# Optimization experiments

Measured on AMD Instinct MI355X. Metric: run time of the kernel, lower is better.

Reference implementation:

```python
import jax, jax.numpy as jnp
import numpy as np

N_LAYERS = 2  # config['layer']
U_, L_, T_, A_ = 200000, 20000, 48, 2000
D_, D3_ = 96, 32
NNZ_ = 2_000_000


def _spmm(rows, cols, vals, x, n_rows):
    # y = A @ x for COO sparse A of shape [n_rows, n_cols]; x: [n_cols, d]
    return jax.ops.segment_sum(vals[:, None] * x[cols], rows, num_segments=n_rows)


def _attn_fuse(z, W1, b1, w2):
    # Attention module: project = Linear(d3,d3)+Tanh+Linear(d3,1, no bias)
    # z: [N, C, d3]; softmax over the C fused channels (dim=1)
    w = jnp.tanh(z @ W1 + b1) @ w2            # [N, C, 1]
    beta = jax.nn.softmax(w, axis=1)
    return jnp.sum(beta * z, axis=1)          # [N, d3]


def setup_inputs() -> dict:
    key = jax.random.key(0)
    ks = iter(jax.random.split(key, 64))
    inp = {}
    inp['user_emb'] = jax.random.normal(next(ks), (U_, D_), jnp.float32) * 0.1
    inp['loc_emb'] = jax.random.normal(next(ks), (L_, D3_), jnp.float32) * 0.1
    inp['time_emb'] = jax.random.normal(next(ks), (T_, D3_), jnp.float32) * 0.1
    inp['act_emb'] = jax.random.normal(next(ks), (A_, D3_), jnp.float32) * 0.1
    for f in ('l', 't', 'a'):
        s = 1.0 / np.sqrt(D3_)
        inp[f'W1_{f}'] = jax.random.normal(next(ks), (D3_, D3_), jnp.float32) * s
        inp[f'b1_{f}'] = jnp.zeros((D3_,), jnp.float32)
        inp[f'w2_{f}'] = jax.random.normal(next(ks), (D3_, 1), jnp.float32) * s

    def add_sparse(prefix, n_rows, n_cols):
        inp[prefix + '_rows'] = jax.random.randint(next(ks), (NNZ_,), 0, n_rows, jnp.int32)
        inp[prefix + '_cols'] = jax.random.randint(next(ks), (NNZ_,), 0, n_cols, jnp.int32)
        inp[prefix + '_vals'] = jax.random.uniform(next(ks), (NNZ_,), jnp.float32) * 0.01

    for p in ('normL', 'normT', 'normA', 'normLT', 'normLA', 'normTA', 'normLTA'):
        add_sparse(p, U_, U_)
    add_sparse('vtoeL', L_, U_)
    add_sparse('vtoeT', T_, U_)
    add_sparse('vtoeA', A_, U_)
    return inp


def reference(user_emb, loc_emb, time_emb, act_emb,
              W1_l, b1_l, w2_l, W1_t, b1_t, w2_t, W1_a, b1_a, w2_a,
              normL_rows, normL_cols, normL_vals,
              normT_rows, normT_cols, normT_vals,
              normA_rows, normA_cols, normA_vals,
              normLT_rows, normLT_cols, normLT_vals,
              normLA_rows, normLA_cols, normLA_vals,
              normTA_rows, normTA_cols, normTA_vals,
              normLTA_rows, normLTA_cols, normLTA_vals,
              vtoeL_rows, vtoeL_cols, vtoeL_vals,
              vtoeT_rows, vtoeT_cols, vtoeT_vals,
              vtoeA_rows, vtoeA_cols, vtoeA_vals):
    U = user_emb.shape[0]
    L, T, A = loc_emb.shape[0], time_emb.shape[0], act_emb.shape[0]
    # disentangle user embedding into 3 factor chunks (torch.split)
    u_l, u_t, u_a = jnp.split(user_emb, 3, axis=-1)
    u_l_all, u_t_all, u_a_all = [u_l], [u_t], [u_a]
    l_e, t_e, a_e = loc_emb, time_emb, act_emb
    l_all, t_all, a_all = [l_e], [t_e], [a_e]
    for _ in range(N_LAYERS):
        # intra-type hypergraph propagation per factor (4 hyperedge types each)
        zl = jnp.stack([
            _spmm(normL_rows, normL_cols, normL_vals, u_l, U),
            _spmm(normLT_rows, normLT_cols, normLT_vals, u_l, U),
            _spmm(normLA_rows, normLA_cols, normLA_vals, u_l, U),
            _spmm(normLTA_rows, normLTA_cols, normLTA_vals, u_l, U)], axis=1)
        zt = jnp.stack([
            _spmm(normT_rows, normT_cols, normT_vals, u_t, U),
            _spmm(normLT_rows, normLT_cols, normLT_vals, u_t, U),
            _spmm(normTA_rows, normTA_cols, normTA_vals, u_t, U),
            _spmm(normLTA_rows, normLTA_cols, normLTA_vals, u_t, U)], axis=1)
        za = jnp.stack([
            _spmm(normA_rows, normA_cols, normA_vals, u_a, U),
            _spmm(normLA_rows, normLA_cols, normLA_vals, u_a, U),
            _spmm(normTA_rows, normTA_cols, normTA_vals, u_a, U),
            _spmm(normLTA_rows, normLTA_cols, normLTA_vals, u_a, U)], axis=1)
        # hyperedge (location/time/activity) updates: vertex -> edge aggregation
        l_e = _spmm(vtoeL_rows, vtoeL_cols, vtoeL_vals, u_l, L)
        t_e = _spmm(vtoeT_rows, vtoeT_cols, vtoeT_vals, u_t, T)
        a_e = _spmm(vtoeA_rows, vtoeA_cols, vtoeA_vals, u_a, A)
        # inter-type attention fusion
        u_l = _attn_fuse(zl, W1_l, b1_l, w2_l)
        u_t = _attn_fuse(zt, W1_t, b1_t, w2_t)
        u_a = _attn_fuse(za, W1_a, b1_a, w2_a)
        u_l_all.append(u_l); u_t_all.append(u_t); u_a_all.append(u_a)
        l_all.append(l_e); t_all.append(t_e); a_all.append(a_e)
    mean = lambda xs: jnp.mean(jnp.stack(xs, 0), 0)
    users = jnp.concatenate([mean(u_l_all), mean(u_t_all), mean(u_a_all)], axis=-1)
    return users, mean(l_all), mean(t_all), mean(a_all)
```

## Files before the change

kernel.cpp:

```cpp
#include <hip/hip_runtime.h>
#include <cmath>

#define U_N 200000
#define L_N 20000
#define T_N 48
#define A_N 2000

#define VAL_SCALE_INV 9.5367431640625e-7f
#define CHUNK 8192
#define BSHIFT_U 6
#define NBUCK_U 3125
#define CAP_U 800
#define BSHIFT_L 3
#define NBUCK_L 2500
#define CAP_LB 1088
#define CAP_AR 1280
#define CAP_TR 44032
#define SL_C 4
#define SA_C 32
#define ST_C 1024
#define THIRD 0.33333333333333333f

__device__ __forceinline__ unsigned short f2bf(float f) {
    unsigned u = __float_as_uint(f);
    return (unsigned short)((u + 0x7FFFu + ((u >> 16) & 1u)) >> 16);
}
__device__ __forceinline__ float bf2f(unsigned short us) {
    return __uint_as_float(((unsigned)us) << 16);
}
__device__ __forceinline__ float blo(unsigned w) { return __uint_as_float(w << 16); }
__device__ __forceinline__ float bhi(unsigned w) { return __uint_as_float(w & 0xFFFF0000u); }
__device__ __forceinline__ float gfma(const unsigned short* __restrict__ x, unsigned e, int lane) {
    float xv = bf2f(x[((size_t)(e >> 14) << 5) + lane]);
    return xv * ((float)(e & 16383u) * VAL_SCALE_INV);
}
__device__ __forceinline__ unsigned quant14(float v) {
    unsigned q = (unsigned)(v * 1048576.0f + 0.5f);
    return q > 16383u ? 16383u : q;
}

__global__ void k_init_users(const float* __restrict__ ue,
                             unsigned short* __restrict__ u_l, unsigned short* __restrict__ u_t,
                             unsigned short* __restrict__ u_a, float* __restrict__ out_users) {
    int i = blockIdx.x * blockDim.x + threadIdx.x;
    if (i >= U_N * 96) return;
    float v = ue[i];
    out_users[i] = v * THIRD;
    int u = i / 96;
    int d = i - u * 96;
    unsigned short b = f2bf(v);
    if (d < 32)       u_l[u * 32 + d]      = b;
    else if (d < 64)  u_t[u * 32 + d - 32] = b;
    else              u_a[u * 32 + d - 64] = b;
}

__global__ void k_seed_edges(const float* __restrict__ le, const float* __restrict__ te,
                             const float* __restrict__ ae,
                             float* __restrict__ ol, float* __restrict__ ot,
                             float* __restrict__ oa) {
    int i = blockIdx.x * blockDim.x + threadIdx.x;
    int nl = L_N * 32, nt = T_N * 32, na = A_N * 32;
    if (i < nl) ol[i] = le[i] * THIRD;
    else if (i < nl + nt) ot[i - nl] = te[i - nl] * THIRD;
    else if (i < nl + nt + na) oa[i - nl - nt] = ae[i - nl - nt] * THIRD;
}

struct CurIni { int* p; int n; int cap; };
struct CurIni10 { CurIni s[10]; };

__global__ void k_cinit(CurIni10 B) {
    CurIni s = B.s[blockIdx.y];
    int i = blockIdx.x * blockDim.x + threadIdx.x;
    if (i < s.n) s.p[i] = i * s.cap;
}

struct USeg { const int* r; const int* c; const float* v; int nnz;
              int bshift; int nbuck; int cap;
              int* bcur; unsigned long long* stage; };
struct UPass { USeg s[3]; int b0[3]; int n; };

__global__ void __launch_bounds__(256) k_passA_multi(UPass P) {
    int b = blockIdx.x;
    int m = 0;
    if (P.n > 1 && b >= P.b0[1]) m = 1;
    if (P.n > 2 && b >= P.b0[2]) m = 2;
    const USeg S = P.s[m];
    int base = (b - P.b0[m]) * CHUNK;
    int n = min(CHUNK, S.nnz - base);
    int t = threadIdx.x;

    __shared__ int cnt[NBUCK_U];
    __shared__ int cur[NBUCK_U];
    for (int i = t; i < S.nbuck; i += 256) cnt[i] = 0;
    __syncthreads();
    for (int i = t; i < n; i += 256)
        atomicAdd(&cnt[S.r[base + i] >> S.bshift], 1);
    __syncthreads();
    for (int bb = t; bb < S.nbuck; bb += 256) {
        int c = cnt[bb];
        cur[bb] = c ? atomicAdd(&S.bcur[bb], c) : 0;
    }
    __syncthreads();
    for (int i = t; i < n; i += 256) {
        int r = S.r[base + i];
        int bkt = r >> S.bshift;
        int p = atomicAdd(&cur[bkt], 1);
        if (p < (bkt + 1) * S.cap)
            S.stage[p] = ((unsigned long long)(unsigned)r << 38) |
                         ((unsigned long long)(unsigned)S.c[base + i] << 14) |
                         quant14(S.v[base + i]);
    }
}

struct FSeg { const unsigned long long* stage; const int* bcur;
              int2* rp2; unsigned* pk; int bshift; int cap; };
struct UFin { FSeg s[3]; int b0[3]; int n; };

__global__ void k_fin_multi(UFin F) {
    int b = blockIdx.x;
    int m = 0;
    if (F.n > 1 && b >= F.b0[1]) m = 1;
    if (F.n > 2 && b >= F.b0[2]) m = 2;
    const FSeg S = F.s[m];
    b -= F.b0[m];
    int t = threadIdx.x;
    int rpb = 1 << S.bshift;
    int rmask = rpb - 1;
    __shared__ int cnt[64];
    __shared__ int lscan[64];
    __shared__ int cur[64];
    __shared__ unsigned pkb[1152];
    int beg = b * S.cap;
    int end = min(S.bcur[b], beg + S.cap);
    int n = end - beg;
    if (t < rpb) cnt[t] = 0;
    __syncthreads();
    for (int e = beg + t; e < end; e += 256)
        atomicAdd(&cnt[(int)(S.stage[e] >> 38) & rmask], 1);
    __syncthreads();
    if (t == 0) {
        int run = 0;
        for (int i = 0; i < rpb; ++i) { lscan[i] = run; run += cnt[i]; }
    }
    __syncthreads();
    int r0 = b << S.bshift;
    if (t < rpb) {
        int s0 = min(lscan[t], S.cap);
        int s1 = min(lscan[t] + cnt[t], S.cap);
        S.rp2[r0 + t] = make_int2(beg + s0, beg + s1);
        cur[t] = lscan[t];
    }
    __syncthreads();
    for (int e = beg + t; e < end; e += 256) {
        unsigned long long v = S.stage[e];
        int p = atomicAdd(&cur[(int)(v >> 38) & rmask], 1);
        pkb[p] = (unsigned)v;
    }
    __syncthreads();
    for (int i = t; i < n; i += 256) S.pk[beg + i] = pkb[i];
}

struct RSeg { const int* r; const int* c; const float* v; int nnz;
              int nrow; int cap; int* bcur; unsigned* gap; };
struct RPass { RSeg s[2]; int b0[2]; int n; };

__global__ void __launch_bounds__(256) k_passR_multi(RPass P) {
    int b = blockIdx.x;
    int m = 0;
    if (P.n > 1 && b >= P.b0[1]) m = 1;
    const RSeg S = P.s[m];
    int base = (b - P.b0[m]) * CHUNK;
    int n = min(CHUNK, S.nnz - base);
    int t = threadIdx.x;
    __shared__ int cnt[2048];
    for (int i = t; i < S.nrow; i += 256) cnt[i] = 0;
    __syncthreads();
    for (int i = t; i < n; i += 256)
        atomicAdd(&cnt[S.r[base + i]], 1);
    __syncthreads();
    for (int rr = t; rr < S.nrow; rr += 256) {
        int c = cnt[rr];
        cnt[rr] = c ? atomicAdd(&S.bcur[rr], c) : 0;
    }
    __syncthreads();
    for (int i = t; i < n; i += 256) {
        int r = S.r[base + i];
        int p = atomicAdd(&cnt[r], 1);
        if (p < (r + 1) * S.cap)
            S.gap[p] = ((unsigned)S.c[base + i] << 14) | quant14(S.v[base + i]);
    }
}

__global__ void __launch_bounds__(256)
k_mega3(const int2* __restrict__ rp0, const unsigned* __restrict__ pk0,
        const int2* __restrict__ rp1, const unsigned* __restrict__ pk1,
        const int2* __restrict__ rp2, const unsigned* __restrict__ pk2,
        const int2* __restrict__ rp3, const unsigned* __restrict__ pk3,
        const unsigned short* __restrict__ x,
        const float* __restrict__ W1, const float* __restrict__ b1,
        const float* __restrict__ w2,
        unsigned short* __restrict__ u_out, float* __restrict__ out_users, int f) {
    __shared__ float sW[1024];
    __shared__ float sb[32];
    __shared__ float sw2[32];
    int t = threadIdx.x;
    for (int i = t; i < 1024; i += 256) sW[i] = W1[i];
    if (t < 32) { sb[t] = b1[t]; sw2[t] = w2[t]; }
    __syncthreads();

    int ch = t & 3;
    int u  = t >> 2;
    int r  = blockIdx.x * 64 + u;

    const int2* rp = (ch == 0) ? rp0 : (ch == 1) ? rp1 : (ch == 2) ? rp2 : rp3;
    const unsigned* pk = (ch == 0) ? pk0 : (ch == 1) ? pk1 : (ch == 2) ? pk2 : pk3;

    float acc[32];
#pragma unroll
    for (int d = 0; d < 32; ++d) acc[d] = 0.f;

    const int2 be = rp[r];
    int j = be.x, end = be.y;
    for (; j < end; j += 2) {
        unsigned e0 = pk[j];
        unsigned e1 = (j + 1 < end) ? pk[j + 1] : 0u;
        float v0 = (float)(e0 & 16383u) * VAL_SCALE_INV;
        float v1 = (j + 1 < end) ? (float)(e1 & 16383u) * VAL_SCALE_INV : 0.f;
        const uint4* xr0 = (const uint4*)(x + ((size_t)(e0 >> 14) << 5));
        const uint4* xr1 = (const uint4*)(x + ((size_t)(e1 >> 14) << 5));
        uint4 A0 = xr0[0], B0 = xr0[1], C0 = xr0[2], D0 = xr0[3];
        uint4 A1 = xr1[0], B1 = xr1[1], C1 = xr1[2], D1 = xr1[3];
#define UPD(wA, wB, base) \
        acc[base]     = fmaf(v0, blo(wA), acc[base]); \
        acc[base]     = fmaf(v1, blo(wB), acc[base]); \
        acc[base + 1] = fmaf(v0, bhi(wA), acc[base + 1]); \
        acc[base + 1] = fmaf(v1, bhi(wB), acc[base + 1]);
        UPD(A0.x, A1.x, 0)  UPD(A0.y, A1.y, 2)  UPD(A0.z, A1.z, 4)  UPD(A0.w, A1.w, 6)
        UPD(B0.x, B1.x, 8)  UPD(B0.y, B1.y, 10) UPD(B0.z, B1.z, 12) UPD(B0.w, B1.w, 14)
        UPD(C0.x, C1.x, 16) UPD(C0.y, C1.y, 18) UPD(C0.z, C1.z, 20) UPD(C0.w, C1.w, 22)
        UPD(D0.x, D1.x, 24) UPD(D0.y, D1.y, 26) UPD(D0.z, D1.z, 28) UPD(D0.w, D1.w, 30)
#undef UPD
    }

    float wsc = 0.f;
#pragma unroll 4
    for (int jj = 0; jj < 32; ++jj) {
        float h = sb[jj];
#pragma unroll
        for (int i = 0; i < 32; ++i) h = fmaf(acc[i], sW[i * 32 + jj], h);
        wsc = fmaf(tanhf(h), sw2[jj], wsc);
    }

    float m = fmaxf(wsc, __shfl_xor(wsc, 1, 4));
    m = fmaxf(m, __shfl_xor(m, 2, 4));
    float e = __expf(wsc - m);
    float s = e + __shfl_xor(e, 1, 4);
    s = s + __shfl_xor(s, 2, 4);
    float beta = e / s;

    float out8[8];
#pragma unroll
    for (int d = 0; d < 32; ++d) {
        float bz = beta * acc[d];
        bz += __shfl_xor(bz, 1, 4);
        bz += __shfl_xor(bz, 2, 4);
        if ((d >> 3) == ch) out8[d & 7] = bz;
    }

    unsigned p0 = (unsigned)f2bf(out8[0]) | ((unsigned)f2bf(out8[1]) << 16);
    unsigned p1 = (unsigned)f2bf(out8[2]) | ((unsigned)f2bf(out8[3]) << 16);
    unsigned p2 = (unsigned)f2bf(out8[4]) | ((unsigned)f2bf(out8[5]) << 16);
    unsigned p3 = (unsigned)f2bf(out8[6]) | ((unsigned)f2bf(out8[7]) << 16);
    *(uint4*)(u_out + (size_t)r * 32 + ch * 8) = make_uint4(p0, p1, p2, p3);

    float4* ou = (float4*)(out_users + (size_t)r * 96 + f * 32 + ch * 8);
    float4 a = ou[0];
    a.x += out8[0] * THIRD; a.y += out8[1] * THIRD;
    a.z += out8[2] * THIRD; a.w += out8[3] * THIRD;
    ou[0] = a;
    float4 b = ou[1];
    b.x += out8[4] * THIRD; b.y += out8[5] * THIRD;
    b.z += out8[6] * THIRD; b.w += out8[7] * THIRD;
    ou[1] = b;
}

__global__ void __launch_bounds__(256)
k_vtoe_rp(const int2* __restrict__ rp2, const unsigned* __restrict__ pk,
          const unsigned short* __restrict__ x, float* __restrict__ out,
          int n_rows, int S) {
    int gid = (blockIdx.x * 256 + threadIdx.x) >> 5;
    int lane = threadIdx.x & 31;
    if (gid >= n_rows * S) return;
    int r = gid / S, s = gid - r * S;
    int2 be = rp2[r];
    int len = be.y - be.x;
    int chunk = (len + S - 1) / S;
    int b = be.x + s * chunk;
    int e = min(be.y, b + chunk);
    if (b >= e) return;
    float a = 0.f;
    int j = b;
    for (; j + 4 <= e; j += 4) {
        unsigned t0 = pk[j], t1 = pk[j + 1], t2 = pk[j + 2], t3 = pk[j + 3];
        a += gfma(x, t0, lane); a += gfma(x, t1, lane);
        a += gfma(x, t2, lane); a += gfma(x, t3, lane);
    }
    for (; j < e; ++j) a += gfma(x, pk[j], lane);
    atomicAdd(&out[(size_t)r * 32 + lane], a * THIRD);
}

__global__ void __launch_bounds__(256)
k_vtoe_gap(const int* __restrict__ bcur, const unsigned* __restrict__ gap,
           int CAP, const unsigned short* __restrict__ x,
           float* __restrict__ out, int n_rows, int S) {
    int gid = (blockIdx.x * 256 + threadIdx.x) >> 5;
    int lane = threadIdx.x & 31;
    if (gid >= n_rows * S) return;
    int r = gid / S, s = gid - r * S;
    int beg = r * CAP;
    int end = min(bcur[r], beg + CAP);
    int len = end - beg;
    int chunk = (len + S - 1) / S;
    int b = beg + s * chunk;
    int e = min(end, b + chunk);
    if (b >= e) return;
    float a = 0.f;
    int j = b;
    for (; j + 4 <= e; j += 4) {
        unsigned t0 = gap[j], t1 = gap[j + 1], t2 = gap[j + 2], t3 = gap[j + 3];
        a += gfma(x, t0, lane); a += gfma(x, t1, lane);
        a += gfma(x, t2, lane); a += gfma(x, t3, lane);
    }
    for (; j < e; ++j) a += gfma(x, gap[j], lane);
    atomicAdd(&out[(size_t)r * 32 + lane], a * THIRD);
}

__global__ void k_init_users_f32(const float* __restrict__ ue,
                                 float* __restrict__ u_l, float* __restrict__ u_t,
                                 float* __restrict__ u_a, float* __restrict__ out_users) {
    int i = blockIdx.x * blockDim.x + threadIdx.x;
    if (i >= U_N * 96) return;
    float v = ue[i];
    out_users[i] = v;
    int u = i / 96;
    int d = i - u * 96;
    if (d < 32)       u_l[u * 32 + d]      = v;
    else if (d < 64)  u_t[u * 32 + d - 32] = v;
    else              u_a[u * 32 + d - 64] = v;
}

__global__ void k_spmm(const int* __restrict__ rows, const int* __restrict__ cols,
                       const float* __restrict__ vals, int nnz,
                       const float* __restrict__ x, float* __restrict__ y) {
    int tid = blockIdx.x * blockDim.x + threadIdx.x;
    int nz = tid >> 5;
    if (nz >= nnz) return;
    int d = tid & 31;
    atomicAdd(&y[(size_t)rows[nz] * 32 + d], vals[nz] * x[(size_t)cols[nz] * 32 + d]);
}

__global__ void k_spmm_smallT(const int* __restrict__ rows, const int* __restrict__ cols,
                              const float* __restrict__ vals, int nnz,
                              const float* __restrict__ x, float* __restrict__ y) {
    __shared__ float acc[T_N * 32];
    for (int i = threadIdx.x; i < T_N * 32; i += blockDim.x) acc[i] = 0.f;
    __syncthreads();
    int d = threadIdx.x & 31;
    int grp = threadIdx.x >> 5;
    int per_block = (nnz + gridDim.x - 1) / gridDim.x;
    int start = blockIdx.x * per_block;
    int end = min(nnz, start + per_block);
    for (int nz = start + grp; nz < end; nz += (blockDim.x >> 5))
        atomicAdd(&acc[rows[nz] * 32 + d], vals[nz] * x[(size_t)cols[nz] * 32 + d]);
    __syncthreads();
    for (int i = threadIdx.x; i < T_N * 32; i += blockDim.x)
        if (acc[i] != 0.f) atomicAdd(&y[i], acc[i]);
}

__global__ void k_attn(const float* __restrict__ z, const float* __restrict__ W1,
                       const float* __restrict__ b1, const float* __restrict__ w2,
                       float* __restrict__ u_out, float* __restrict__ out_users, int f) {
    __shared__ float sW[32 * 32];
    __shared__ float sb[32];
    __shared__ float sw2[32];
    for (int i = threadIdx.x; i < 1024; i += blockDim.x) sW[i] = W1[i];
    if (threadIdx.x < 32) { sb[threadIdx.x] = b1[threadIdx.x]; sw2[threadIdx.x] = w2[threadIdx.x]; }
    __syncthreads();
    int half = threadIdx.x >> 5;
    int j = threadIdx.x & 31;
    int u = blockIdx.x * 8 + half;
    if (u >= U_N) return;
    float zk[4];
#pragma unroll
    for (int k = 0; k < 4; ++k) zk[k] = z[(size_t)k * (U_N * 32) + (size_t)u * 32 + j];
    float w[4];
#pragma unroll
    for (int k = 0; k < 4; ++k) {
        float h = sb[j];
#pragma unroll
        for (int i = 0; i < 32; ++i) h += __shfl(zk[k], i, 32) * sW[i * 32 + j];
        float p = tanhf(h) * sw2[j];
#pragma unroll
        for (int off = 16; off; off >>= 1) p += __shfl_xor(p, off, 32);
        w[k] = p;
    }
    float m = fmaxf(fmaxf(w[0], w[1]), fmaxf(w[2], w[3]));
    float e0 = __expf(w[0] - m), e1 = __expf(w[1] - m), e2 = __expf(w[2] - m), e3 = __expf(w[3] - m);
    float inv = 1.f / (e0 + e1 + e2 + e3);
    float o = (e0 * zk[0] + e1 * zk[1] + e2 * zk[2] + e3 * zk[3]) * inv;
    u_out[(size_t)u * 32 + j] = o;
    out_users[(size_t)u * 96 + f * 32 + j] += o;
}

__global__ void k_scale(float* __restrict__ out, int n) {
    int i = blockIdx.x * blockDim.x + threadIdx.x;
    if (i < n) out[i] *= (1.0f / 3.0f);
}

extern "C" void kernel_launch(void* const* d_in, const int* in_sizes, int n_in,
                              void* d_out, int out_size, void* d_ws, size_t ws_size,
                              hipStream_t stream) {
    const float* user_emb = (const float*)d_in[0];
    const float* loc_emb  = (const float*)d_in[1];
    const float* time_emb = (const float*)d_in[2];
    const float* act_emb  = (const float*)d_in[3];
    const float* W1s[3] = {(const float*)d_in[4], (const float*)d_in[7], (const float*)d_in[10]};
    const float* b1s[3] = {(const float*)d_in[5], (const float*)d_in[8], (const float*)d_in[11]};
    const float* w2s[3] = {(const float*)d_in[6], (const float*)d_in[9], (const float*)d_in[12]};

    struct Mat { const int* r; const int* c; const float* v; int nnz; int nrows; };
    auto mk = [&](int base, int nrows) {
        return Mat{(const int*)d_in[base], (const int*)d_in[base + 1],
                   (const float*)d_in[base + 2], in_sizes[base], nrows};
    };
    Mat M[10] = {mk(13, U_N), mk(16, U_N), mk(19, U_N), mk(22, U_N), mk(25, U_N),
                 mk(28, U_N), mk(31, U_N), mk(34, L_N), mk(37, T_N), mk(40, A_N)};

    float* out       = (float*)d_out;
    float* out_users = out;
    float* out_l     = out + (size_t)U_N * 96;
    float* out_t     = out_l + (size_t)L_N * 32;
    float* out_a     = out_t + (size_t)T_N * 32;

    const int chmat[3][4] = {{0, 3, 4, 6}, {1, 3, 5, 6}, {2, 4, 5, 6}};

    auto align256 = [](size_t x) { return (x + 255) & ~(size_t)255; };
    char* wsb = (char*)d_ws;
    size_t off = 0;
    size_t ubuf_off[4];
    for (int b = 0; b < 4; ++b) { ubuf_off[b] = off; off = align256(off + (size_t)U_N * 32 * 2); }
    size_t rp2_off[7], pk_off[7], bcurU_off[7];
    for (int b = 0; b < 7; ++b) { rp2_off[b] = off; off = align256(off + (size_t)U_N * 8); }
    for (int b = 0; b < 7; ++b) { bcurU_off[b] = off; off = align256(off + (size_t)NBUCK_U * 4); }
    for (int b = 0; b < 7; ++b) { pk_off[b] = off; off = align256(off + (size_t)NBUCK_U * CAP_U * 4); }
    size_t rp2L_off = off; off = align256(off + (size_t)L_N * 8);
    size_t bcurL_off = off; off = align256(off + (size_t)NBUCK_L * 4);
    size_t pkL_off  = off; off = align256(off + (size_t)NBUCK_L * CAP_LB * 4);
    size_t bcurA_off = off; off = align256(off + (size_t)A_N * 4);
    size_t bcurT_off = off; off = align256(off + (size_t)T_N * 4);
    size_t gapA_bytes = (size_t)A_N * CAP_AR * 4;
    size_t gapT_bytes = (size_t)T_N * CAP_TR * 4;
    size_t stageU_bytes = (size_t)NBUCK_U * CAP_U * 8;
    size_t s2_bytes = align256(gapA_bytes) + align256(gapT_bytes);
    if (s2_bytes < stageU_bytes) s2_bytes = stageU_bytes;
    size_t s2_off = off; off = align256(off + s2_bytes);
    size_t stageL_bytes = (size_t)NBUCK_L * CAP_LB * 8;
    size_t s1_bytes = (stageU_bytes > stageL_bytes) ? stageU_bytes : stageL_bytes;
    size_t s1_off = off; off = align256(off + s1_bytes);
    size_t NEED = off;

    if (ws_size >= NEED) {
        unsigned long long* stg1 = (unsigned long long*)(wsb + s1_off);
        unsigned long long* stg2 = (unsigned long long*)(wsb + s2_off);
        unsigned long long* stg3 = (unsigned long long*)(wsb + pk_off[4]);
        int* bcurL = (int*)(wsb + bcurL_off);
        int* bcurA = (int*)(wsb + bcurA_off);
        int* bcurT = (int*)(wsb + bcurT_off);
        unsigned* gapA = (unsigned*)(wsb + s2_off);
        unsigned* gapT = (unsigned*)(wsb + s2_off + align256(gapA_bytes));

        CurIni10 B;
        for (int b = 0; b < 7; ++b)
            B.s[b] = CurIni{(int*)(wsb + bcurU_off[b]), NBUCK_U, CAP_U};
        B.s[7] = CurIni{bcurL, NBUCK_L, CAP_LB};
        B.s[8] = CurIni{bcurA, A_N, CAP_AR};
        B.s[9] = CurIni{bcurT, T_N, CAP_TR};
        k_cinit<<<dim3((NBUCK_U + 255) / 256, 10), 256, 0, stream>>>(B);

        unsigned short* bufs[4];
        for (int b = 0; b < 4; ++b) bufs[b] = (unsigned short*)(wsb + ubuf_off[b]);
        k_init_users<<<(U_N * 96 + 255) / 256, 256, 0, stream>>>(
            user_emb, bufs[0], bufs[1], bufs[2], out_users);
        int nseed = (L_N + T_N + A_N) * 32;
        k_seed_edges<<<(nseed + 255) / 256, 256, 0, stream>>>(
            loc_emb, time_emb, act_emb, out_l, out_t, out_a);

        unsigned long long* stgs[3] = {stg1, stg2, stg3};
        auto runPhase = [&](const int* mats, int n) {
            UPass P; P.n = n;
            int blk = 0;
            for (int k = 0; k < n; ++k) {
                int m = mats[k];
                P.s[k] = USeg{M[m].r, M[m].c, M[m].v, M[m].nnz,
                              BSHIFT_U, NBUCK_U, CAP_U,
                              (int*)(wsb + bcurU_off[m]), stgs[k]};
                P.b0[k] = blk;
                blk += (M[m].nnz + CHUNK - 1) / CHUNK;
            }
            k_passA_multi<<<blk, 256, 0, stream>>>(P);
            UFin F; F.n = n;
            for (int k = 0; k < n; ++k) {
                int m = mats[k];
                F.s[k] = FSeg{stgs[k], (const int*)(wsb + bcurU_off[m]),
                              (int2*)(wsb + rp2_off[m]), (unsigned*)(wsb + pk_off[m]),
                              BSHIFT_U, CAP_U};
                F.b0[k] = k * NBUCK_U;
            }
            k_fin_multi<<<n * NBUCK_U, 256, 0, stream>>>(F);
        };
        const int ph1[3] = {0, 1, 2};
        const int ph2[2] = {3, 4};
        const int ph3[2] = {5, 6};
        runPhase(ph1, 3);
        runPhase(ph2, 2);
        runPhase(ph3, 2);

        {
            UPass P; P.n = 1;
            P.s[0] = USeg{M[7].r, M[7].c, M[7].v, M[7].nnz,
                          BSHIFT_L, NBUCK_L, CAP_LB, bcurL, stg1};
            P.b0[0] = 0;
            k_passA_multi<<<(M[7].nnz + CHUNK - 1) / CHUNK, 256, 0, stream>>>(P);
            UFin F; F.n = 1;
            F.s[0] = FSeg{stg1, bcurL, (int2*)(wsb + rp2L_off),
                          (unsigned*)(wsb + pkL_off), BSHIFT_L, CAP_LB};
            F.b0[0] = 0;
            k_fin_multi<<<NBUCK_L, 256, 0, stream>>>(F);
        }

        {
            RPass P; P.n = 2;
            P.s[0] = RSeg{M[9].r, M[9].c, M[9].v, M[9].nnz, A_N, CAP_AR, bcurA, gapA};
            P.b0[0] = 0;
            int blk = (M[9].nnz + CHUNK - 1) / CHUNK;
            P.s[1] = RSeg{M[8].r, M[8].c, M[8].v, M[8].nnz, T_N, CAP_TR, bcurT, gapT};
            P.b0[1] = blk;
            blk += (M[8].nnz + CHUNK - 1) / CHUNK;
            k_passR_multi<<<blk, 256, 0, stream>>>(P);
        }

        unsigned short* ucur[3] = {bufs[0], bufs[1], bufs[2]};
        unsigned short* uspare = bufs[3];
        auto rpP = [&](int b) { return (const int2*)(wsb + rp2_off[b]); };
        auto pkP = [&](int b) { return (const unsigned*)(wsb + pk_off[b]); };

        for (int f = 0; f < 3; ++f) {
            const int* cm = chmat[f];
            for (int layer = 0; layer < 2; ++layer) {
                if (f == 0)
                    k_vtoe_rp<<<((size_t)L_N * SL_C * 32 + 255) / 256, 256, 0, stream>>>(
                        (const int2*)(wsb + rp2L_off), (const unsigned*)(wsb + pkL_off),
                        ucur[0], out_l, L_N, SL_C);
                else if (f == 1)
                    k_vtoe_gap<<<((size_t)T_N * ST_C * 32 + 255) / 256, 256, 0, stream>>>(
                        bcurT, gapT, CAP_TR, ucur[1], out_t, T_N, ST_C);
                else
                    k_vtoe_gap<<<((size_t)A_N * SA_C * 32 + 255) / 256, 256, 0, stream>>>(
                        bcurA, gapA, CAP_AR, ucur[2], out_a, A_N, SA_C);
                k_mega3<<<NBUCK_U, 256, 0, stream>>>(
                    rpP(cm[0]), pkP(cm[0]), rpP(cm[1]), pkP(cm[1]),
                    rpP(cm[2]), pkP(cm[2]), rpP(cm[3]), pkP(cm[3]),
                    ucur[f], W1s[f], b1s[f], w2s[f], uspare, out_users, f);
                unsigned short* t = ucur[f]; ucur[f] = uspare; uspare = t;
            }
        }
    } else {
        float* ws = (float*)d_ws;
        float* z = ws;
        float* u[3];
        u[0] = ws + (size_t)4 * U_N * 32;
        u[1] = u[0] + (size_t)U_N * 32;
        u[2] = u[1] + (size_t)U_N * 32;
        k_init_users_f32<<<(U_N * 96 + 255) / 256, 256, 0, stream>>>(
            user_emb, u[0], u[1], u[2], out_users);
        hipMemcpyAsync(out_l, loc_emb,  (size_t)L_N * 32 * 4, hipMemcpyDeviceToDevice, stream);
        hipMemcpyAsync(out_t, time_emb, (size_t)T_N * 32 * 4, hipMemcpyDeviceToDevice, stream);
        hipMemcpyAsync(out_a, act_emb,  (size_t)A_N * 32 * 4, hipMemcpyDeviceToDevice, stream);
        float* oute[3] = {out_l, out_t, out_a};
        for (int layer = 0; layer < 2; ++layer) {
            for (int f = 0; f < 3; ++f) {
                hipMemsetAsync(z, 0, (size_t)4 * U_N * 32 * 4, stream);
                for (int k = 0; k < 4; ++k) {
                    Mat& m = M[chmat[f][k]];
                    k_spmm<<<((size_t)m.nnz * 32 + 255) / 256, 256, 0, stream>>>(
                        m.r, m.c, m.v, m.nnz, u[f], z + (size_t)k * U_N * 32);
                }
                Mat& vm = M[7 + f];
                if (f == 1)
                    k_spmm_smallT<<<2048, 256, 0, stream>>>(vm.r, vm.c, vm.v, vm.nnz, u[f], oute[f]);
                else
                    k_spmm<<<((size_t)vm.nnz * 32 + 255) / 256, 256, 0, stream>>>(
                        vm.r, vm.c, vm.v, vm.nnz, u[f], oute[f]);
                k_attn<<<(U_N + 7) / 8, 256, 0, stream>>>(z, W1s[f], b1s[f], w2s[f], u[f], out_users, f);
            }
        }
        int total = U_N * 96 + L_N * 32 + T_N * 32 + A_N * 32;
        k_scale<<<(total + 255) / 256, 256, 0, stream>>>(out, total);
    }
}
```

Measured before the change: 2.140 ms.

## Restructure vertex-to-edge kernels to one thread per slice with register accumulators

The vtoe kernels change from a 32-lane group per row slice (one lane per feature) to one thread per slice that gathers whole 64-byte bf16 rows into 32 register accumulators, reusing the mega3 inner loop as a shared helper. Groups of four adjacent threads reduce their partials with shuffles, and each thread then issues eight atomic adds. This removes 32x redundant index loads and scalar per-lane gathers and aims for wider vector loads. In exchange the launch has far fewer threads, each thread carries higher register pressure and serial work, and the shuffle reduction assumes that S is a multiple of 4 so that the four lanes of a group share the same row.

```diff
diff --git a/kernel.cpp b/kernel.cpp
--- a/kernel.cpp
+++ b/kernel.cpp
@@ -191,6 +191,31 @@
     }
 }
 
+#define UPD(wA, wB, base) \
+        acc[base]     = fmaf(v0, blo(wA), acc[base]); \
+        acc[base]     = fmaf(v1, blo(wB), acc[base]); \
+        acc[base + 1] = fmaf(v0, bhi(wA), acc[base + 1]); \
+        acc[base + 1] = fmaf(v1, bhi(wB), acc[base + 1]);
+
+__device__ __forceinline__ void acc_span(float* acc, const unsigned* __restrict__ pk,
+                                         int j, int end,
+                                         const unsigned short* __restrict__ x) {
+    for (; j < end; j += 2) {
+        unsigned e0 = pk[j];
+        unsigned e1 = (j + 1 < end) ? pk[j + 1] : 0u;
+        float v0 = (float)(e0 & 16383u) * VAL_SCALE_INV;
+        float v1 = (j + 1 < end) ? (float)(e1 & 16383u) * VAL_SCALE_INV : 0.f;
+        const uint4* xr0 = (const uint4*)(x + ((size_t)(e0 >> 14) << 5));
+        const uint4* xr1 = (const uint4*)(x + ((size_t)(e1 >> 14) << 5));
+        uint4 A0 = xr0[0], B0 = xr0[1], C0 = xr0[2], D0 = xr0[3];
+        uint4 A1 = xr1[0], B1 = xr1[1], C1 = xr1[2], D1 = xr1[3];
+        UPD(A0.x, A1.x, 0)  UPD(A0.y, A1.y, 2)  UPD(A0.z, A1.z, 4)  UPD(A0.w, A1.w, 6)
+        UPD(B0.x, B1.x, 8)  UPD(B0.y, B1.y, 10) UPD(B0.z, B1.z, 12) UPD(B0.w, B1.w, 14)
+        UPD(C0.x, C1.x, 16) UPD(C0.y, C1.y, 18) UPD(C0.z, C1.z, 20) UPD(C0.w, C1.w, 22)
+        UPD(D0.x, D1.x, 24) UPD(D0.y, D1.y, 26) UPD(D0.z, D1.z, 28) UPD(D0.w, D1.w, 30)
+    }
+}
+
 __global__ void __launch_bounds__(256)
 k_mega3(const int2* __restrict__ rp0, const unsigned* __restrict__ pk0,
         const int2* __restrict__ rp1, const unsigned* __restrict__ pk1,
@@ -220,27 +245,7 @@
     for (int d = 0; d < 32; ++d) acc[d] = 0.f;
 
     const int2 be = rp[r];
-    int j = be.x, end = be.y;
-    for (; j < end; j += 2) {
-        unsigned e0 = pk[j];
-        unsigned e1 = (j + 1 < end) ? pk[j + 1] : 0u;
-        float v0 = (float)(e0 & 16383u) * VAL_SCALE_INV;
-        float v1 = (j + 1 < end) ? (float)(e1 & 16383u) * VAL_SCALE_INV : 0.f;
-        const uint4* xr0 = (const uint4*)(x + ((size_t)(e0 >> 14) << 5));
-        const uint4* xr1 = (const uint4*)(x + ((size_t)(e1 >> 14) << 5));
-        uint4 A0 = xr0[0], B0 = xr0[1], C0 = xr0[2], D0 = xr0[3];
-        uint4 A1 = xr1[0], B1 = xr1[1], C1 = xr1[2], D1 = xr1[3];
-#define UPD(wA, wB, base) \
-        acc[base]     = fmaf(v0, blo(wA), acc[base]); \
-        acc[base]     = fmaf(v1, blo(wB), acc[base]); \
-        acc[base + 1] = fmaf(v0, bhi(wA), acc[base + 1]); \
-        acc[base + 1] = fmaf(v1, bhi(wB), acc[base + 1]);
-        UPD(A0.x, A1.x, 0)  UPD(A0.y, A1.y, 2)  UPD(A0.z, A1.z, 4)  UPD(A0.w, A1.w, 6)
-        UPD(B0.x, B1.x, 8)  UPD(B0.y, B1.y, 10) UPD(B0.z, B1.z, 12) UPD(B0.w, B1.w, 14)
-        UPD(C0.x, C1.x, 16) UPD(C0.y, C1.y, 18) UPD(C0.z, C1.z, 20) UPD(C0.w, C1.w, 22)
-        UPD(D0.x, D1.x, 24) UPD(D0.y, D1.y, 26) UPD(D0.z, D1.z, 28) UPD(D0.w, D1.w, 30)
-#undef UPD
-    }
+    acc_span(acc, pk, be.x, be.y, x);
 
     float wsc = 0.f;
 #pragma unroll 4
@@ -284,12 +289,25 @@
     ou[1] = b;
 }
 
+__device__ __forceinline__ void vtoe_epilogue(float* acc, float* out, int r, int q) {
+    float out8[8];
+#pragma unroll
+    for (int d = 0; d < 32; ++d) {
+        float bz = acc[d];
+        bz += __shfl_xor(bz, 1, 4);
+        bz += __shfl_xor(bz, 2, 4);
+        if ((d >> 3) == q) out8[d & 7] = bz;
+    }
+#pragma unroll
+    for (int k = 0; k < 8; ++k)
+        atomicAdd(&out[(size_t)r * 32 + q * 8 + k], out8[k] * THIRD);
+}
+
 __global__ void __launch_bounds__(256)
 k_vtoe_rp(const int2* __restrict__ rp2, const unsigned* __restrict__ pk,
           const unsigned short* __restrict__ x, float* __restrict__ out,
           int n_rows, int S) {
-    int gid = (blockIdx.x * 256 + threadIdx.x) >> 5;
-    int lane = threadIdx.x & 31;
+    int gid = blockIdx.x * 256 + threadIdx.x;
     if (gid >= n_rows * S) return;
     int r = gid / S, s = gid - r * S;
     int2 be = rp2[r];
@@ -297,24 +315,18 @@
     int chunk = (len + S - 1) / S;
     int b = be.x + s * chunk;
     int e = min(be.y, b + chunk);
-    if (b >= e) return;
-    float a = 0.f;
-    int j = b;
-    for (; j + 4 <= e; j += 4) {
-        unsigned t0 = pk[j], t1 = pk[j + 1], t2 = pk[j + 2], t3 = pk[j + 3];
-        a += gfma(x, t0, lane); a += gfma(x, t1, lane);
-        a += gfma(x, t2, lane); a += gfma(x, t3, lane);
-    }
-    for (; j < e; ++j) a += gfma(x, pk[j], lane);
-    atomicAdd(&out[(size_t)r * 32 + lane], a * THIRD);
+    float acc[32];
+#pragma unroll
+    for (int d = 0; d < 32; ++d) acc[d] = 0.f;
+    if (b < e) acc_span(acc, pk, b, e, x);
+    vtoe_epilogue(acc, out, r, threadIdx.x & 3);
 }
 
 __global__ void __launch_bounds__(256)
 k_vtoe_gap(const int* __restrict__ bcur, const unsigned* __restrict__ gap,
            int CAP, const unsigned short* __restrict__ x,
            float* __restrict__ out, int n_rows, int S) {
-    int gid = (blockIdx.x * 256 + threadIdx.x) >> 5;
-    int lane = threadIdx.x & 31;
+    int gid = blockIdx.x * 256 + threadIdx.x;
     if (gid >= n_rows * S) return;
     int r = gid / S, s = gid - r * S;
     int beg = r * CAP;
@@ -323,16 +335,11 @@
     int chunk = (len + S - 1) / S;
     int b = beg + s * chunk;
     int e = min(end, b + chunk);
-    if (b >= e) return;
-    float a = 0.f;
-    int j = b;
-    for (; j + 4 <= e; j += 4) {
-        unsigned t0 = gap[j], t1 = gap[j + 1], t2 = gap[j + 2], t3 = gap[j + 3];
-        a += gfma(x, t0, lane); a += gfma(x, t1, lane);
-        a += gfma(x, t2, lane); a += gfma(x, t3, lane);
-    }
-    for (; j < e; ++j) a += gfma(x, gap[j], lane);
-    atomicAdd(&out[(size_t)r * 32 + lane], a * THIRD);
+    float acc[32];
+#pragma unroll
+    for (int d = 0; d < 32; ++d) acc[d] = 0.f;
+    if (b < e) acc_span(acc, gap, b, e, x);
+    vtoe_epilogue(acc, out, r, threadIdx.x & 3);
 }
 
 __global__ void k_init_users_f32(const float* __restrict__ ue,
@@ -558,14 +565,14 @@
             const int* cm = chmat[f];
             for (int layer = 0; layer < 2; ++layer) {
                 if (f == 0)
-                    k_vtoe_rp<<<((size_t)L_N * SL_C * 32 + 255) / 256, 256, 0, stream>>>(
+                    k_vtoe_rp<<<((size_t)L_N * SL_C + 255) / 256, 256, 0, stream>>>(
                         (const int2*)(wsb + rp2L_off), (const unsigned*)(wsb + pkL_off),
                         ucur[0], out_l, L_N, SL_C);
                 else if (f == 1)
-                    k_vtoe_gap<<<((size_t)T_N * ST_C * 32 + 255) / 256, 256, 0, stream>>>(
+                    k_vtoe_gap<<<((size_t)T_N * ST_C + 255) / 256, 256, 0, stream>>>(
                         bcurT, gapT, CAP_TR, ucur[1], out_t, T_N, ST_C);
                 else
-                    k_vtoe_gap<<<((size_t)A_N * SA_C * 32 + 255) / 256, 256, 0, stream>>>(
+                    k_vtoe_gap<<<((size_t)A_N * SA_C + 255) / 256, 256, 0, stream>>>(
                         bcurA, gapA, CAP_AR, ucur[2], out_a, A_N, SA_C);
                 k_mega3<<<NBUCK_U, 256, 0, stream>>>(
                     rpP(cm[0]), pkP(cm[0]), rpP(cm[1]), pkP(cm[1]),
```

Measured after the change: 2.328 ms. 1.09x slower.
